# Kernel tuning notes

Hardware: AMD Instinct MI355X
Metric: run time of the kernel (lower is better)

Reference implementation:

```python
import jax, jax.numpy as jnp
from jax import lax
import numpy as np

EPS = 1e-5  # BatchNorm2d default eps

def _cbs(x, w, g, b, m, v, pad):
    # Conv2d(bias=False) + BatchNorm2d (eval mode, running stats) + SiLU
    y = lax.conv_general_dilated(x, w, (1, 1), [(pad, pad), (pad, pad)],
                                 dimension_numbers=('NCHW', 'OIHW', 'NCHW'))
    y = (y - m[None, :, None, None]) * (g / jnp.sqrt(v + EPS))[None, :, None, None] + b[None, :, None, None]
    return y * jax.nn.sigmoid(y)

def setup_inputs():
    key = jax.random.key(0)
    B, C1, C2, H, W = 2, 128, 128, 20, 20
    ks = iter(jax.random.split(key, 16))
    def wconv(o, i, s):
        return jax.random.normal(next(ks), (o, i, s, s), jnp.float32) / np.float32(np.sqrt(i * s * s))
    def bn(cdim):
        k1, k2 = jax.random.split(next(ks))
        g = jax.random.uniform(k1, (cdim,), jnp.float32, 0.5, 1.5)
        b = jax.random.normal(k2, (cdim,), jnp.float32) * 0.1
        return g, b, jnp.zeros((cdim,), jnp.float32), jnp.ones((cdim,), jnp.float32)
    inp = {'x': jax.random.normal(next(ks), (B, C1, H, W), jnp.float32)}
    inp['w1'] = wconv(C2, C1, 1); inp['g1'], inp['b1'], inp['m1'], inp['v1'] = bn(C2)
    inp['w2'] = wconv(C2, C1, 1); inp['g2'], inp['b2'], inp['m2'], inp['v2'] = bn(C2)
    inp['wr1'] = wconv(C2, 2 * C2, 1); inp['gr1'], inp['br1'], inp['mr1'], inp['vr1'] = bn(C2)
    inp['wr2'] = wconv(C2, C2, 3); inp['gr2'], inp['br2'], inp['mr2'], inp['vr2'] = bn(C2)
    inp['wr3'] = wconv(1, C2, 1); inp['gr3'], inp['br3'], inp['mr3'], inp['vr3'] = bn(1)
    return inp

def reference(x, w1, g1, b1, m1, v1, w2, g2, b2, m2, v2,
              wr1, gr1, br1, mr1, vr1, wr2, gr2, br2, mr2, vr2,
              wr3, gr3, br3, mr3, vr3):
    B, C, H, W = x.shape
    HW = H * W
    # feat: [B, HW, C2]
    feat = _cbs(x, w1, g1, b1, m1, v1, 0).reshape(B, -1, HW).transpose(0, 2, 1)
    C2 = feat.shape[-1]
    # pairwise concat: rel[b,i,j] = [feat[b,i], feat[b,j]]  -> [B, HW, HW, 2*C2]
    fi = jnp.broadcast_to(feat[:, :, None, :], (B, HW, HW, C2))
    fj = jnp.broadcast_to(feat[:, None, :, :], (B, HW, HW, C2))
    rel = jnp.concatenate([fi, fj], axis=-1)
    # faithful permute(0,3,1,2) + contiguous view to [B*HW, 2*C2, H, W]
    rel = rel.transpose(0, 3, 1, 2).reshape(B * HW, 2 * C2, H, W)
    r = _cbs(rel, wr1, gr1, br1, mr1, vr1, 0)
    r = _cbs(r, wr2, gr2, br2, mr2, vr2, 1)
    r = _cbs(r, wr3, gr3, br3, mr3, vr3, 0)  # [B*HW, 1, H, W]
    scores = r.reshape(B, HW, HW)
    # bmm aggregation then back to [B, C2, H, W]
    att = jnp.einsum('bij,bjc->bic', scores, feat).transpose(0, 2, 1).reshape(B, C2, H, W)
    return _cbs(att, w2, g2, b2, m2, v2, 0) + x
```

## Files before the change

kernel.cpp:

```cpp
#include <hip/hip_runtime.h>

#define EPS 1e-5f

typedef __bf16 bf16x8 __attribute__((ext_vector_type(8)));
typedef float  f32x4  __attribute__((ext_vector_type(4)));

__device__ __forceinline__ unsigned short f2bf(float f) {
  unsigned int u = __float_as_uint(f);
  unsigned int r = (u + 0x7fffu + ((u >> 16) & 1u)) >> 16;
  return (unsigned short)r;
}
__device__ __forceinline__ float silu(float y) { return y / (1.f + __expf(-y)); }

__global__ void prep_kernel(const float* __restrict__ x, const float* __restrict__ w1,
                            const float* __restrict__ g1, const float* __restrict__ b1,
                            const float* __restrict__ m1, const float* __restrict__ v1,
                            const float* __restrict__ wr2, const float* __restrict__ wr1,
                            float* __restrict__ feat, float* __restrict__ attz,
                            unsigned short* __restrict__ Apack, float* __restrict__ Pfx,
                            float* __restrict__ Wt, float* __restrict__ featsum) {
  int blk = blockIdx.x;
  int tid = threadIdx.x;
  if (blk < 400) {
    int hp = tid >> 7, c = tid & 127;
    int pp = blk * 2 + hp;
    int b = pp / 400, p = pp % 400;
    __shared__ float xv[2][128];
    xv[hp][c] = x[(b * 128 + c) * 400 + p];
    __syncthreads();
    const float4* w4 = (const float4*)(w1 + c * 128);
    const float4* v4 = (const float4*)xv[hp];
    float s0 = 0.f, s1 = 0.f, s2 = 0.f, s3 = 0.f;
#pragma unroll
    for (int i = 0; i < 32; ++i) {
      float4 wv = w4[i], xx = v4[i];
      s0 += wv.x * xx.x; s1 += wv.y * xx.y; s2 += wv.z * xx.z; s3 += wv.w * xx.w;
    }
    float s = (s0 + s1) + (s2 + s3);
    float sc = g1[c] * rsqrtf(v1[c] + EPS);
    float y = s * sc + (b1[c] - m1[c] * sc);
    int o = (b * 400 + p) * 128 + c;
    feat[o] = silu(y);
    if (p >= 200) attz[o] = 0.f;
  } else if (blk < 472) {
    int f = (blk - 400) * 4 + (tid >> 6);
    int lane = tid & 63;
    int tap = f >> 5, ks = (f >> 3) & 3, m8 = f & 7;
    int o  = m8 * 16 + (lane & 15);
    int cb = ks * 32 + (lane >> 4) * 8;
    unsigned short* dst = Apack + ((size_t)f * 64 + lane) * 8;
#pragma unroll
    for (int j = 0; j < 8; ++j)
      dst[j] = f2bf(wr2[(o * 128 + (cb + j)) * 9 + tap]);
  } else if (blk == 472) {
    if (tid < 128) {
      float s = 0.f;
      float* Po = Pfx + tid * 257;
      Po[0] = 0.f;
      for (int k = 0; k < 256; ++k) { s += wr1[tid * 256 + k]; Po[k + 1] = s; }
    }
    for (int k = tid; k < 2304; k += 256) featsum[k] = 0.f;
  } else {
    int base = (blk - 473) * 1024;
#pragma unroll
    for (int k = 0; k < 4; ++k) {
      int idx = base + k * 256 + tid;
      int tap = idx >> 14;
      int r = idx & 16383;
      int i = r >> 7, o = r & 127;
      Wt[idx] = wr2[(o * 128 + i) * 9 + tap];
    }
  }
}

__global__ void featsum_kernel(const float* __restrict__ feat, float* __restrict__ featsum) {
  int bi = blockIdx.x; int b = bi >> 2, quarter = bi & 3;
  int c = threadIdx.x;
  float s[9];
#pragma unroll
  for (int k = 0; k < 9; ++k) s[k] = 0.f;
  for (int p = quarter * 100; p < quarter * 100 + 100; ++p) {
    int r = p / 20, cm = p - 20 * r;
    int ry = (r == 0) ? 0 : (r == 19) ? 2 : 1;
    int rx = (cm == 0) ? 0 : (cm == 19) ? 2 : 1;
    int pat = ry * 3 + rx;
    float v = feat[(b * 400 + p) * 128 + c];
#pragma unroll
    for (int k = 0; k < 9; ++k) s[k] += (k == pat) ? v : 0.f;
  }
#pragma unroll
  for (int k = 0; k < 9; ++k) atomicAdd(&featsum[(b * 9 + k) * 128 + c], s[k]);
}

__global__ __launch_bounds__(512, 4) void rel_kernel(
    const float* __restrict__ feat, const float* __restrict__ wr1, const float* __restrict__ Pfx,
    const float* __restrict__ gr1, const float* __restrict__ br1,
    const float* __restrict__ mr1, const float* __restrict__ vr1,
    const unsigned short* __restrict__ Apack, const float* __restrict__ Wt,
    const float* __restrict__ featsum,
    const float* __restrict__ gr2, const float* __restrict__ br2,
    const float* __restrict__ mr2, const float* __restrict__ vr2,
    const float* __restrict__ wr3,
    const float* __restrict__ gr3, const float* __restrict__ br3,
    const float* __restrict__ mr3, const float* __restrict__ vr3,
    float* __restrict__ att) {

  __shared__ __align__(16) unsigned short r1f[16 * 221 * 8];
  __shared__ float f0s[220], f1s[220], scoreS[208];
  __shared__ float wB0s[128], wB1s[128];
  __shared__ float sc1[128], sh1[128], sc2[128], sh2[128], w3c[128];
  __shared__ float attT[128];
  __shared__ float fA[256], r1c[128], AvS[128];
  __shared__ float vS[9 * 128];
  __shared__ float spS[9];

  int tid = threadIdx.x, lane = tid & 63, wid = tid >> 6;
  int blk = blockIdx.x;

  if (tid < 128) {
    float s1 = gr1[tid] * rsqrtf(vr1[tid] + EPS); sc1[tid] = s1; sh1[tid] = br1[tid] - mr1[tid] * s1;
    float s2 = gr2[tid] * rsqrtf(vr2[tid] + EPS); sc2[tid] = s2; sh2[tid] = br2[tid] - mr2[tid] * s2;
    w3c[tid] = wr3[tid];
    attT[tid] = 0.f; AvS[tid] = 0.f;
  }
  float s3 = gr3[0] * rsqrtf(vr3[0] + EPS);
  float sh3 = br3[0] - mr3[0] * s3;

  if (blk < 800) {
    int idx = blk >> 1, half = blk & 1;
    int b = idx / 200, q = 200 + idx % 200;
    int c0 = (q * 256) / 400, c1 = c0 + 1;
    if (tid < 128) {
      const float* Po = Pfx + tid * 257;
      int e0 = min(256, 400 * c0 + 400 - 256 * q);
      wB0s[tid] = Po[e0];
      float wv = 0.f;
      if (c1 < 256) {
        int s1i = min(256, max(0, 400 * c1 - 256 * q));
        wv = Po[256] - Po[s1i];
      }
      wB1s[tid] = wv;
    }
    if (tid < 220) {
      int p = tid + 180 * half;
      f0s[tid] = feat[(b * 400 + p) * 128 + (c0 - 128)];
      f1s[tid] = (c1 < 256) ? feat[(b * 400 + p) * 128 + (c1 - 128)] : 0.f;
    }
    if (tid < 208) scoreS[tid] = 0.f;
    __syncthreads();

    for (int i = tid; i < 3520; i += 512) {
      int plane = i / 220, p = i - plane * 220;
      int cb = (plane >> 2) * 32 + (plane & 3) * 8;
      float fa0 = f0s[p], fa1 = f1s[p];
      unsigned int pk[4];
#pragma unroll
      for (int jp = 0; jp < 4; ++jp) {
        int c = cb + jp * 2;
        float y0 = wB0s[c] * fa0 + wB1s[c] * fa1;     y0 = y0 * sc1[c] + sh1[c];
        float y1 = wB0s[c + 1] * fa0 + wB1s[c + 1] * fa1; y1 = y1 * sc1[c + 1] + sh1[c + 1];
        pk[jp] = (unsigned int)f2bf(silu(y0)) | ((unsigned int)f2bf(silu(y1)) << 16);
      }
      *(uint4*)&r1f[(plane * 221 + p) * 8] = make_uint4(pk[0], pk[1], pk[2], pk[3]);
    }
    if (tid < 16) *(uint4*)&r1f[(tid * 221 + 220) * 8] = make_uint4(0, 0, 0, 0);

    int wm = wid & 1, wn = wid >> 1;
    int ntcnt = (wn == 0) ? 4 : 3;
    int n16 = lane & 15, quad = lane >> 4;
    int hA[4], wA[4], poA[4]; bool pov[4];
#pragma unroll
    for (int t = 0; t < 4; ++t) {
      int po = (wn + 4 * t) * 16 + n16;
      poA[t] = po; pov[t] = po < 200;
      int pg = half * 200 + po;
      hA[t] = pg / 20; wA[t] = pg - 20 * hA[t];
    }
    f32x4 acc[4][4];
#pragma unroll
    for (int mt = 0; mt < 4; ++mt)
#pragma unroll
      for (int t = 0; t < 4; ++t) acc[mt][t] = f32x4{0.f, 0.f, 0.f, 0.f};

    __syncthreads();

    const char* wbase = (const char*)Apack + (size_t)((wm * 4) * 64 + lane) * 16;
    for (int tap = 0; tap < 9; ++tap) {
      int dy = tap / 3 - 1, dx = tap % 3 - 1;
      int pp[4];
#pragma unroll
      for (int t = 0; t < 4; ++t) {
        int hh = hA[t] + dy, ww = wA[t] + dx;
        bool valid = pov[t] & (hh >= 0) & (hh < 20) & (ww >= 0) & (ww < 20);
        pp[t] = valid ? (hh - 9 * half) * 20 + ww : 220;
      }
#pragma unroll
      for (int ks = 0; ks < 4; ++ks) {
        const char* wp = wbase + (size_t)(tap * 4 + ks) * 8192;
        bf16x8 af0 = *(const bf16x8*)(wp);
        bf16x8 af1 = *(const bf16x8*)(wp + 1024);
        bf16x8 af2 = *(const bf16x8*)(wp + 2048);
        bf16x8 af3 = *(const bf16x8*)(wp + 3072);
        int pbase = (ks * 4 + quad) * 221;
#pragma unroll
        for (int t = 0; t < 4; ++t) {
          if (t < ntcnt) {
            bf16x8 bfr = *(const bf16x8*)&r1f[(pbase + pp[t]) * 8];
            acc[0][t] = __builtin_amdgcn_mfma_f32_16x16x32_bf16(af0, bfr, acc[0][t], 0, 0, 0);
            acc[1][t] = __builtin_amdgcn_mfma_f32_16x16x32_bf16(af1, bfr, acc[1][t], 0, 0, 0);
            acc[2][t] = __builtin_amdgcn_mfma_f32_16x16x32_bf16(af2, bfr, acc[2][t], 0, 0, 0);
            acc[3][t] = __builtin_amdgcn_mfma_f32_16x16x32_bf16(af3, bfr, acc[3][t], 0, 0, 0);
          }
        }
      }
    }

#pragma unroll
    for (int t = 0; t < 4; ++t) {
      if (t < ntcnt) {
        float ps = 0.f;
#pragma unroll
        for (int mt = 0; mt < 4; ++mt) {
#pragma unroll
          for (int r = 0; r < 4; ++r) {
            int o = wm * 64 + mt * 16 + quad * 4 + r;
            float y = acc[mt][t][r] * sc2[o] + sh2[o];
            ps += silu(y) * w3c[o];
          }
        }
        ps += __shfl_xor(ps, 16);
        ps += __shfl_xor(ps, 32);
        if (quad == 0 && pov[t]) atomicAdd(&scoreS[poA[t]], ps);
      }
    }
    __syncthreads();

    if (tid < 200) scoreS[tid] = silu(scoreS[tid] * s3 + sh3);
    __syncthreads();

    {
      int c = tid & 127, part = tid >> 7;
      float s = 0.f;
      int j0 = part * 50;
      for (int j = j0; j < j0 + 50; ++j)
        s += scoreS[j] * feat[(b * 400 + half * 200 + j) * 128 + c];
      atomicAdd(&attT[c], s);
    }
    __syncthreads();
    if (tid < 128)
      atomicAdd(&att[((size_t)(b * 400 + q)) * 128 + tid], attT[tid]);
  } else {
    int cidx = blk - 800;
    int b = cidx / 200, q = cidx % 200;
    if (tid < 256) {
      int u = q * 256 + tid; int c = u / 400, i2 = u - c * 400;
      fA[tid] = feat[(b * 400 + i2) * 128 + c];
    }
    for (int k = tid; k < 1152; k += 512) vS[k] = 0.f;
    __syncthreads();
    {
      int o = tid & 127, part = tid >> 7;
      const float* wr = wr1 + o * 256 + part * 64;
      const float* fv = fA + part * 64;
      float a = 0.f;
#pragma unroll 8
      for (int k = 0; k < 64; ++k) a += wr[k] * fv[k];
      atomicAdd(&AvS[o], a);
    }
    __syncthreads();
    if (tid < 128) r1c[tid] = silu(AvS[tid] * sc1[tid] + sh1[tid]);
    __syncthreads();
    {
      int o = tid & 127, part = tid >> 7;
      const float* rc = r1c + part * 32;
      for (int tap = 0; tap < 9; ++tap) {
        const float* wt = Wt + tap * 16384 + part * 32 * 128 + o;
        float s = 0.f;
#pragma unroll 8
        for (int i2 = 0; i2 < 32; ++i2) s += wt[i2 * 128] * rc[i2];
        atomicAdd(&vS[tap * 128 + o], s);
      }
    }
    __syncthreads();
    for (int pat = wid; pat < 9; pat += 8) {
      int ry = pat / 3, rx = pat % 3;
      float ps = 0.f;
      for (int oo = lane; oo < 128; oo += 64) {
        float y = 0.f;
#pragma unroll
        for (int dy = -1; dy <= 1; ++dy) {
          if ((ry == 0 && dy < 0) || (ry == 2 && dy > 0)) continue;
#pragma unroll
          for (int dx = -1; dx <= 1; ++dx) {
            if ((rx == 0 && dx < 0) || (rx == 2 && dx > 0)) continue;
            y += vS[((dy + 1) * 3 + (dx + 1)) * 128 + oo];
          }
        }
        y = y * sc2[oo] + sh2[oo];
        ps += silu(y) * w3c[oo];
      }
#pragma unroll
      for (int sft = 32; sft >= 1; sft >>= 1) ps += __shfl_xor(ps, sft);
      if (lane == 0) spS[pat] = silu(ps * s3 + sh3);
    }
    __syncthreads();
    if (tid < 128) {
      float a = 0.f;
#pragma unroll
      for (int pat = 0; pat < 9; ++pat) a += spS[pat] * featsum[(b * 9 + pat) * 128 + tid];
      att[((size_t)(b * 400 + q)) * 128 + tid] = a;
    }
  }
}

__global__ void out_kernel(const float* __restrict__ att, const float* __restrict__ x,
                           const float* __restrict__ w2,
                           const float* __restrict__ g2, const float* __restrict__ b2,
                           const float* __restrict__ m2, const float* __restrict__ v2,
                           float* __restrict__ out) {
  int blk = blockIdx.x;
  int tid = threadIdx.x;
  int hp = tid >> 7, c = tid & 127;
  int pp = blk * 2 + hp;
  int b = pp / 400, p = pp % 400;
  __shared__ float av[2][128];
  av[hp][c] = att[(size_t)(b * 400 + p) * 128 + c];
  __syncthreads();
  const float4* w4 = (const float4*)(w2 + c * 128);
  const float4* v4 = (const float4*)av[hp];
  float s0 = 0.f, s1 = 0.f, s2 = 0.f, s3 = 0.f;
#pragma unroll
  for (int i = 0; i < 32; ++i) {
    float4 wv = w4[i], xx = v4[i];
    s0 += wv.x * xx.x; s1 += wv.y * xx.y; s2 += wv.z * xx.z; s3 += wv.w * xx.w;
  }
  float s = (s0 + s1) + (s2 + s3);
  float sc = g2[c] * rsqrtf(v2[c] + EPS);
  float y = s * sc + (b2[c] - m2[c] * sc);
  int xi = (b * 128 + c) * 400 + p;
  out[xi] = silu(y) + x[xi];
}

extern "C" void kernel_launch(void* const* d_in, const int* in_sizes, int n_in,
                              void* d_out, int out_size, void* d_ws, size_t ws_size,
                              hipStream_t stream) {
  const float* x   = (const float*)d_in[0];
  const float* w1  = (const float*)d_in[1];
  const float* g1  = (const float*)d_in[2];
  const float* b1  = (const float*)d_in[3];
  const float* m1  = (const float*)d_in[4];
  const float* v1  = (const float*)d_in[5];
  const float* w2  = (const float*)d_in[6];
  const float* g2  = (const float*)d_in[7];
  const float* b2  = (const float*)d_in[8];
  const float* m2  = (const float*)d_in[9];
  const float* v2  = (const float*)d_in[10];
  const float* wr1 = (const float*)d_in[11];
  const float* gr1 = (const float*)d_in[12];
  const float* br1 = (const float*)d_in[13];
  const float* mr1 = (const float*)d_in[14];
  const float* vr1 = (const float*)d_in[15];
  const float* wr2 = (const float*)d_in[16];
  const float* gr2 = (const float*)d_in[17];
  const float* br2 = (const float*)d_in[18];
  const float* mr2 = (const float*)d_in[19];
  const float* vr2 = (const float*)d_in[20];
  const float* wr3 = (const float*)d_in[21];
  const float* gr3 = (const float*)d_in[22];
  const float* br3 = (const float*)d_in[23];
  const float* mr3 = (const float*)d_in[24];
  const float* vr3 = (const float*)d_in[25];
  float* out = (float*)d_out;

  char* ws = (char*)d_ws;
  float*          feat    = (float*)ws;
  float*          attb    = (float*)(ws + 409600);
  unsigned short* Apack   = (unsigned short*)(ws + 819200);
  float*          Pfx     = (float*)(ws + 1114112);
  float*          Wt      = (float*)(ws + 1245696);
  float*          featsum = (float*)(ws + 1835520);

  prep_kernel<<<617, 256, 0, stream>>>(x, w1, g1, b1, m1, v1, wr2, wr1,
                                       feat, attb, Apack, Pfx, Wt, featsum);
  featsum_kernel<<<8, 128, 0, stream>>>(feat, featsum);
  rel_kernel<<<1200, 512, 0, stream>>>(feat, wr1, Pfx, gr1, br1, mr1, vr1,
                                       Apack, Wt, featsum,
                                       gr2, br2, mr2, vr2, wr3, gr3, br3, mr3, vr3, attb);
  out_kernel<<<400, 256, 0, stream>>>(attb, x, w2, g2, b2, m2, v2, out);
}
```

Before: 232.0 us.

## Drop featsum kernel, parallelize prefix sums, and split out_kernel dot products

Removes the separate featsum_kernel launch. Affected rel_kernel blocks now compute the aggregation directly by expanding the 9 pattern scores to 400 positions and reducing over feat with shared atomics. The Pfx prefix sum, formerly a serial loop in a single block, becomes a wavefront shuffle scan spread over 32 blocks. out_kernel now uses one block per position, with two threads per channel combined via shuffle. This trades a launch and a serial tail for extra per-block work: each tail block of rel_kernel rereads 400x128 of feat.

```diff
diff --git a/kernel.cpp b/kernel.cpp
--- a/kernel.cpp
+++ b/kernel.cpp
@@ -18,7 +18,7 @@
                             const float* __restrict__ wr2, const float* __restrict__ wr1,
                             float* __restrict__ feat, float* __restrict__ attz,
                             unsigned short* __restrict__ Apack, float* __restrict__ Pfx,
-                            float* __restrict__ Wt, float* __restrict__ featsum) {
+                            float* __restrict__ Wt) {
   int blk = blockIdx.x;
   int tid = threadIdx.x;
   if (blk < 400) {
@@ -52,16 +52,26 @@
 #pragma unroll
     for (int j = 0; j < 8; ++j)
       dst[j] = f2bf(wr2[(o * 128 + (cb + j)) * 9 + tap]);
-  } else if (blk == 472) {
-    if (tid < 128) {
-      float s = 0.f;
-      float* Po = Pfx + tid * 257;
-      Po[0] = 0.f;
-      for (int k = 0; k < 256; ++k) { s += wr1[tid * 256 + k]; Po[k + 1] = s; }
-    }
-    for (int k = tid; k < 2304; k += 256) featsum[k] = 0.f;
+  } else if (blk < 504) {
+    int o = (blk - 472) * 4 + (tid >> 6);
+    int lane = tid & 63;
+    float4 wv = ((const float4*)(wr1 + o * 256))[lane];
+    float p0 = wv.x, p1 = p0 + wv.y, p2 = p1 + wv.z, p3 = p2 + wv.w;
+    float v = p3;
+#pragma unroll
+    for (int d = 1; d < 64; d <<= 1) {
+      float t = __shfl_up(v, d);
+      if (lane >= d) v += t;
+    }
+    float off = v - p3;
+    float* Po = Pfx + o * 257;
+    if (lane == 0) Po[0] = 0.f;
+    Po[lane * 4 + 1] = off + p0;
+    Po[lane * 4 + 2] = off + p1;
+    Po[lane * 4 + 3] = off + p2;
+    Po[lane * 4 + 4] = off + p3;
   } else {
-    int base = (blk - 473) * 1024;
+    int base = (blk - 504) * 1024;
 #pragma unroll
     for (int k = 0; k < 4; ++k) {
       int idx = base + k * 256 + tid;
@@ -73,31 +83,11 @@
   }
 }
 
-__global__ void featsum_kernel(const float* __restrict__ feat, float* __restrict__ featsum) {
-  int bi = blockIdx.x; int b = bi >> 2, quarter = bi & 3;
-  int c = threadIdx.x;
-  float s[9];
-#pragma unroll
-  for (int k = 0; k < 9; ++k) s[k] = 0.f;
-  for (int p = quarter * 100; p < quarter * 100 + 100; ++p) {
-    int r = p / 20, cm = p - 20 * r;
-    int ry = (r == 0) ? 0 : (r == 19) ? 2 : 1;
-    int rx = (cm == 0) ? 0 : (cm == 19) ? 2 : 1;
-    int pat = ry * 3 + rx;
-    float v = feat[(b * 400 + p) * 128 + c];
-#pragma unroll
-    for (int k = 0; k < 9; ++k) s[k] += (k == pat) ? v : 0.f;
-  }
-#pragma unroll
-  for (int k = 0; k < 9; ++k) atomicAdd(&featsum[(b * 9 + k) * 128 + c], s[k]);
-}
-
 __global__ __launch_bounds__(512, 4) void rel_kernel(
     const float* __restrict__ feat, const float* __restrict__ wr1, const float* __restrict__ Pfx,
     const float* __restrict__ gr1, const float* __restrict__ br1,
     const float* __restrict__ mr1, const float* __restrict__ vr1,
     const unsigned short* __restrict__ Apack, const float* __restrict__ Wt,
-    const float* __restrict__ featsum,
     const float* __restrict__ gr2, const float* __restrict__ br2,
     const float* __restrict__ mr2, const float* __restrict__ vr2,
     const float* __restrict__ wr3,
@@ -113,6 +103,7 @@
   __shared__ float fA[256], r1c[128], AvS[128];
   __shared__ float vS[9 * 128];
   __shared__ float spS[9];
+  __shared__ float spP[400];
 
   int tid = threadIdx.x, lane = tid & 63, wid = tid >> 6;
   int blk = blockIdx.x;
@@ -304,12 +295,25 @@
       if (lane == 0) spS[pat] = silu(ps * s3 + sh3);
     }
     __syncthreads();
-    if (tid < 128) {
-      float a = 0.f;
-#pragma unroll
-      for (int pat = 0; pat < 9; ++pat) a += spS[pat] * featsum[(b * 9 + pat) * 128 + tid];
-      att[((size_t)(b * 400 + q)) * 128 + tid] = a;
-    }
+
+    for (int p = tid; p < 400; p += 512) {
+      int r = p / 20, cm = p - 20 * r;
+      int ry = (r == 0) ? 0 : (r == 19) ? 2 : 1;
+      int rx = (cm == 0) ? 0 : (cm == 19) ? 2 : 1;
+      spP[p] = spS[ry * 3 + rx];
+    }
+    __syncthreads();
+    {
+      int c = tid & 127, part = tid >> 7;
+      const float* fb = feat + ((size_t)(b * 400) + part * 100) * 128 + c;
+      const float* sp = spP + part * 100;
+      float s = 0.f;
+      for (int j = 0; j < 100; ++j) s += sp[j] * fb[(size_t)j * 128];
+      atomicAdd(&attT[c], s);
+    }
+    __syncthreads();
+    if (tid < 128)
+      att[((size_t)(b * 400 + q)) * 128 + tid] = attT[tid];
   }
 }
 
@@ -318,27 +322,29 @@
                            const float* __restrict__ g2, const float* __restrict__ b2,
                            const float* __restrict__ m2, const float* __restrict__ v2,
                            float* __restrict__ out) {
-  int blk = blockIdx.x;
+  int pp = blockIdx.x;
+  int b = pp / 400, p = pp % 400;
   int tid = threadIdx.x;
-  int hp = tid >> 7, c = tid & 127;
-  int pp = blk * 2 + hp;
-  int b = pp / 400, p = pp % 400;
-  __shared__ float av[2][128];
-  av[hp][c] = att[(size_t)(b * 400 + p) * 128 + c];
+  __shared__ float av[128];
+  if (tid < 128) av[tid] = att[(size_t)(b * 400 + p) * 128 + tid];
   __syncthreads();
-  const float4* w4 = (const float4*)(w2 + c * 128);
-  const float4* v4 = (const float4*)av[hp];
+  int c = tid >> 1, part = tid & 1;
+  const float4* w4 = (const float4*)(w2 + c * 128 + part * 64);
+  const float4* v4 = (const float4*)(av + part * 64);
   float s0 = 0.f, s1 = 0.f, s2 = 0.f, s3 = 0.f;
 #pragma unroll
-  for (int i = 0; i < 32; ++i) {
+  for (int i = 0; i < 16; ++i) {
     float4 wv = w4[i], xx = v4[i];
     s0 += wv.x * xx.x; s1 += wv.y * xx.y; s2 += wv.z * xx.z; s3 += wv.w * xx.w;
   }
   float s = (s0 + s1) + (s2 + s3);
-  float sc = g2[c] * rsqrtf(v2[c] + EPS);
-  float y = s * sc + (b2[c] - m2[c] * sc);
-  int xi = (b * 128 + c) * 400 + p;
-  out[xi] = silu(y) + x[xi];
+  s += __shfl_xor(s, 1);
+  if (part == 0) {
+    float sc = g2[c] * rsqrtf(v2[c] + EPS);
+    float y = s * sc + (b2[c] - m2[c] * sc);
+    int xi = (b * 128 + c) * 400 + p;
+    out[xi] = silu(y) + x[xi];
+  }
 }
 
 extern "C" void kernel_launch(void* const* d_in, const int* in_sizes, int n_in,
@@ -373,18 +379,16 @@
   float* out = (float*)d_out;
 
   char* ws = (char*)d_ws;
-  float*          feat    = (float*)ws;
-  float*          attb    = (float*)(ws + 409600);
-  unsigned short* Apack   = (unsigned short*)(ws + 819200);
-  float*          Pfx     = (float*)(ws + 1114112);
-  float*          Wt      = (float*)(ws + 1245696);
-  float*          featsum = (float*)(ws + 1835520);
-
-  prep_kernel<<<617, 256, 0, stream>>>(x, w1, g1, b1, m1, v1, wr2, wr1,
-                                       feat, attb, Apack, Pfx, Wt, featsum);
-  featsum_kernel<<<8, 128, 0, stream>>>(feat, featsum);
+  float*          feat  = (float*)ws;
+  float*          attb  = (float*)(ws + 409600);
+  unsigned short* Apack = (unsigned short*)(ws + 819200);
+  float*          Pfx   = (float*)(ws + 1114112);
+  float*          Wt    = (float*)(ws + 1245696);
+
+  prep_kernel<<<648, 256, 0, stream>>>(x, w1, g1, b1, m1, v1, wr2, wr1,
+                                       feat, attb, Apack, Pfx, Wt);
   rel_kernel<<<1200, 512, 0, stream>>>(feat, wr1, Pfx, gr1, br1, mr1, vr1,
-                                       Apack, Wt, featsum,
+                                       Apack, Wt,
                                        gr2, br2, mr2, vr2, wr3, gr3, br3, mr3, vr3, attb);
-  out_kernel<<<400, 256, 0, stream>>>(attb, x, w2, g2, b2, m2, v2, out);
-}
+  out_kernel<<<800, 256, 0, stream>>>(attb, x, w2, g2, b2, m2, v2, out);
+}
```

Result: faster. 213.5 us (-8.0%).
